# Optimization experiments

Hardware: AMD Instinct MI355X
Metric: run time of the kernel (lower is better)

Reference implementation:

```python
import jax, jax.numpy as jnp
import numpy as np

# Per-level grid spatial shapes: ceil([T,H,W]/grid_size/2**i) + 1 with
# video (T,H,W) = (120,1080,1920), grid_size=8, n_levels=2.
GRID_SHAPES = [jnp.array([16.0, 136.0, 241.0], dtype=jnp.float32),
               jnp.array([9.0, 69.0, 121.0], dtype=jnp.float32)]
EMB_DIM = 16
N_PTS = 1_000_000

# 8 binary corner offsets, MSB-first bit order (matches f'{i:03b}').
OFFSETS = jnp.array([[(i >> 2) & 1, (i >> 1) & 1, i & 1] for i in range(8)],
                    dtype=jnp.float32)  # [8,3]


def setup_inputs() -> dict:
    key = jax.random.key(0)
    k0, k1, k2 = jax.random.split(key, 3)
    inputs = jax.random.uniform(k0, (N_PTS, 3), dtype=jnp.float32)
    emb0 = jax.random.normal(k1, (16, 136, 241, EMB_DIM), dtype=jnp.float32)
    emb1 = jax.random.normal(k2, (9, 69, 121, EMB_DIM), dtype=jnp.float32)
    return {"inputs": inputs, "emb0": emb0, "emb1": emb1}


def _encode_level(inputs, emb, gshape):
    # inputs: [N,3] in [0,1]; emb: [T,H,W,D]; gshape: [3] float grid shape
    coords = inputs * (gshape - 1.0)                         # [N,3]
    corner = jnp.floor(coords[:, None, :] + OFFSETS)         # [N,8,3]
    corner = jnp.clip(corner, 0.0, gshape - 1.0)             # [N,8,3]
    idx = corner.astype(jnp.int32)
    values = emb[idx[..., 0], idx[..., 1], idx[..., 2]]      # [N,8,D] gather
    weights = jnp.prod(1.0 - jnp.abs(corner - coords[:, None, :]),
                       axis=-1, keepdims=True)               # [N,8,1]
    return jnp.sum(weights * values, axis=-2)                # [N,D]


def reference(inputs, emb0, emb1):
    out0 = _encode_level(inputs, emb0, GRID_SHAPES[0])
    out1 = _encode_level(inputs, emb1, GRID_SHAPES[1])
    return jnp.concatenate([out0, out1], axis=-1)            # [N, 2*D]
```

## Files before the change

kernel.cpp:

```cpp
#include <hip/hip_runtime.h>


typedef float floatx4 __attribute__((ext_vector_type(4)));

#define KXB 8
#define KYB 17
#define KZB 31
#define NBINS (KXB * KYB * KZB)
#define NSUB 4
#define CAPS 104
#define CAP_TOT (NSUB * CAPS)

#define L0X 3
#define L0Y 9
#define L0Z 9
#define L0CELLS (L0X * L0Y * L0Z)
#define L1X 3
#define L1Y 6
#define L1Z 5
#define L1CELLS (L1X * L1Y * L1Z)
#define CSTR 20

__device__ __forceinline__ int point_key(float px, float py, float pz) {
    int ix = (int)(px * 15.0f);  ix = min(max(ix, 0), 15);
    int iy = (int)(py * 135.0f); iy = min(max(iy, 0), 135);
    int iz = (int)(pz * 240.0f); iz = min(max(iz, 0), 240);
    return ((ix >> 1) * KYB + (iy >> 3)) * KZB + (iz >> 3);
}

__device__ __forceinline__ void load4pts(const float* __restrict__ pts, int i4,
                                         float px[4], float py[4], float pz[4]) {
    const floatx4* v = (const floatx4*)(pts + (size_t)i4 * 3);
    const floatx4 a = v[0], b = v[1], c = v[2];
    px[0] = a.x; py[0] = a.y; pz[0] = a.z;
    px[1] = a.w; py[1] = b.x; pz[1] = b.y;
    px[2] = b.z; py[2] = b.w; pz[2] = c.x;
    px[3] = c.y; py[3] = c.z; pz[3] = c.w;
}

__global__ __launch_bounds__(256)
void k_bin(const float* __restrict__ pts, int n,
           unsigned* __restrict__ cnt, unsigned* __restrict__ ovfc,
           unsigned* __restrict__ slots, unsigned* __restrict__ ovf) {
    const int i4 = (blockIdx.x * blockDim.x + threadIdx.x) * 4;
    if (i4 >= n) return;
    if (i4 + 3 < n) {
        float px[4], py[4], pz[4];
        load4pts(pts, i4, px, py, pz);
        int k[4];
#pragma unroll
        for (int j = 0; j < 4; ++j) k[j] = point_key(px[j], py[j], pz[j]);
        unsigned pos[4];
#pragma unroll
        for (int j = 0; j < 4; ++j)
            pos[j] = atomicAdd(&cnt[j * NBINS + k[j]], 1u);
#pragma unroll
        for (int j = 0; j < 4; ++j) {
            if (pos[j] < CAPS)
                slots[(size_t)k[j] * CAP_TOT + j * CAPS + pos[j]] = (unsigned)(i4 + j);
            else
                ovf[atomicAdd(ovfc, 1u)] = (unsigned)(i4 + j);
        }
    } else {
        for (int j = 0; j < 4 && i4 + j < n; ++j) {
            const size_t b = (size_t)(i4 + j) * 3;
            const int k = point_key(pts[b], pts[b+1], pts[b+2]);
            const unsigned pos = atomicAdd(&cnt[j * NBINS + k], 1u);
            if (pos < CAPS) slots[(size_t)k * CAP_TOT + j * CAPS + pos] = (unsigned)(i4 + j);
            else            ovf[atomicAdd(ovfc, 1u)] = (unsigned)(i4 + j);
        }
    }
}

__device__ __forceinline__ void setup_lds(float cx, float cy, float cz,
                                          float tm1, float hm1, float wm1,
                                          int xb, int yb, int zb,
                                          int ex, int ey, int ez,
                                          int sx, int sy, int d,
                                          int* __restrict__ off,
                                          float* __restrict__ w) {
    float gx[2] = { floorf(cx), floorf(cx + 1.0f) };
    float gy[2] = { floorf(cy), floorf(cy + 1.0f) };
    float gz[2] = { floorf(cz), floorf(cz + 1.0f) };
    float wx[2], wy[2], wz[2];
    int   xo[2], yo[2], zo[2];
#pragma unroll
    for (int b = 0; b < 2; ++b) {
        gx[b] = fminf(fmaxf(gx[b], 0.0f), tm1);
        gy[b] = fminf(fmaxf(gy[b], 0.0f), hm1);
        gz[b] = fminf(fmaxf(gz[b], 0.0f), wm1);
        wx[b] = 1.0f - fabsf(gx[b] - cx);
        wy[b] = 1.0f - fabsf(gy[b] - cy);
        wz[b] = 1.0f - fabsf(gz[b] - cz);
        xo[b] = min((int)gx[b] - xb, ex) * sx;
        yo[b] = min((int)gy[b] - yb, ey) * sy;
        zo[b] = min((int)gz[b] - zb, ez) * CSTR + d;
    }
    float wyz[4];
    int   yzo[4];
#pragma unroll
    for (int j = 0; j < 2; ++j)
#pragma unroll
        for (int k = 0; k < 2; ++k) {
            wyz[2 * j + k] = wy[j] * wz[k];
            yzo[2 * j + k] = yo[j] + zo[k];
        }
#pragma unroll
    for (int c = 0; c < 8; ++c) {
        const int i = (c >> 2) & 1, jk = c & 3;
        w[c]   = wx[i] * wyz[jk];
        off[c] = xo[i] + yzo[jk];
    }
}

__global__ __launch_bounds__(256)
void k_main_bins(const unsigned* __restrict__ slots,
                 const unsigned* __restrict__ cnt,
                 const float* __restrict__ pts,
                 const float* __restrict__ emb0,
                 const float* __restrict__ emb1,
                 float* __restrict__ out) {
    const int bin = (blockIdx.x & 7) * 527 + (blockIdx.x >> 3);
    const unsigned n0 = min(cnt[bin],             (unsigned)CAPS);
    const unsigned n1 = min(cnt[NBINS + bin],     (unsigned)CAPS);
    const unsigned n2 = min(cnt[2 * NBINS + bin], (unsigned)CAPS);
    const unsigned n3 = min(cnt[3 * NBINS + bin], (unsigned)CAPS);
    const unsigned c0 = n0, c1 = c0 + n1, c2 = c1 + n2, nt = c2 + n3;
    if (nt == 0) return;

    const int bz = bin % KZB;
    const int t1 = bin / KZB;
    const int by = t1 % KYB;
    const int bx = t1 / KYB;

    const int x0 = bx * 2, y0 = by * 8, z0 = bz * 8;
    const int x1b = bx, y1b = (544 * by) / 135, z1b = bz * 4;

    __shared__ float lds0[L0CELLS * CSTR];
    __shared__ float lds1[L1CELLS * CSTR];

    const int tid = threadIdx.x;
    for (int idx = tid; idx < L0CELLS * 4; idx += 256) {
        const int cell = idx >> 2, q = (idx & 3) * 4;
        const int lz = cell % L0Z;
        const int t = cell / L0Z;
        const int ly = t % L0Y, lx = t / L0Y;
        const int gx = min(x0 + lx, 15), gy = min(y0 + ly, 135), gz = min(z0 + lz, 240);
        const floatx4 v = *(const floatx4*)(emb0 + ((size_t)(gx * 136 + gy) * 241 + gz) * 16 + q);
        *(floatx4*)(lds0 + cell * CSTR + q) = v;
    }
    for (int idx = tid; idx < L1CELLS * 4; idx += 256) {
        const int cell = idx >> 2, q = (idx & 3) * 4;
        const int lz = cell % L1Z;
        const int t = cell / L1Z;
        const int ly = t % L1Y, lx = t / L1Y;
        const int gx = min(x1b + lx, 8), gy = min(y1b + ly, 68), gz = min(z1b + lz, 120);
        const floatx4 v = *(const floatx4*)(emb1 + ((size_t)(gx * 69 + gy) * 121 + gz) * 16 + q);
        *(floatx4*)(lds1 + cell * CSTR + q) = v;
    }
    __syncthreads();

    const int quad = tid >> 2;
    const int d = (tid & 3) * 4;
    const size_t sbase = (size_t)bin * CAP_TOT;

    auto slot_of = [&](unsigned t) -> unsigned {
        const unsigned seg = (t >= c0) + (t >= c1) + (t >= c2);
        const unsigned base = (seg == 0) ? 0u : ((seg == 1) ? c0 : ((seg == 2) ? c1 : c2));
        return (unsigned)(sbase + seg * CAPS + (t - base));
    };

    unsigned tA = quad, tB = quad + 64;
    int origA = (int)slots[slot_of(min(tA, nt - 1))];
    int origB = (int)slots[slot_of(min(tB, nt - 1))];
    size_t pbA = (size_t)origA * 3;
    float pxA = pts[pbA], pyA = pts[pbA + 1], pzA = pts[pbA + 2];

    while (tA < nt) {
        const unsigned tC = tB + 64;
        const int origC = (int)slots[slot_of(min(tC, nt - 1))];
        const size_t pbB = (size_t)origB * 3;
        const float pxB = pts[pbB], pyB = pts[pbB + 1], pzB = pts[pbB + 2];

        int   o0[8], o1[8];
        float w0[8], w1[8];
        setup_lds(pxA * 15.0f, pyA * 135.0f, pzA * 240.0f, 15.0f, 135.0f, 240.0f,
                  x0, y0, z0, L0X - 1, L0Y - 1, L0Z - 1,
                  L0Y * L0Z * CSTR, L0Z * CSTR, d, o0, w0);
        setup_lds(pxA * 8.0f, pyA * 68.0f, pzA * 120.0f, 8.0f, 68.0f, 120.0f,
                  x1b, y1b, z1b, L1X - 1, L1Y - 1, L1Z - 1,
                  L1Y * L1Z * CSTR, L1Z * CSTR, d, o1, w1);

        floatx4 a0 = {0.f, 0.f, 0.f, 0.f}, a1 = {0.f, 0.f, 0.f, 0.f};
#pragma unroll
        for (int c = 0; c < 8; ++c) a0 += w0[c] * *(const floatx4*)(lds0 + o0[c]);
#pragma unroll
        for (int c = 0; c < 8; ++c) a1 += w1[c] * *(const floatx4*)(lds1 + o1[c]);

        float* row = out + (size_t)origA * 32 + d;
        __builtin_nontemporal_store(a0, (floatx4*)row);
        __builtin_nontemporal_store(a1, (floatx4*)(row + 16));

        tA = tB; tB = tC;
        origA = origB; origB = origC;
        pxA = pxB; pyA = pyB; pzA = pzB;
    }
}

__device__ __forceinline__ void setup_glb(float cx, float cy, float cz,
                                          float tm1, float hm1, float wm1,
                                          int sh, int sw, int d,
                                          int* __restrict__ off,
                                          float* __restrict__ w) {
    float gx[2] = { floorf(cx), floorf(cx + 1.0f) };
    float gy[2] = { floorf(cy), floorf(cy + 1.0f) };
    float gz[2] = { floorf(cz), floorf(cz + 1.0f) };
    float wx[2], wy[2], wz[2];
    int   xo[2], yo[2], zo[2];
#pragma unroll
    for (int b = 0; b < 2; ++b) {
        gx[b] = fminf(fmaxf(gx[b], 0.0f), tm1);
        gy[b] = fminf(fmaxf(gy[b], 0.0f), hm1);
        gz[b] = fminf(fmaxf(gz[b], 0.0f), wm1);
        wx[b] = 1.0f - fabsf(gx[b] - cx);
        wy[b] = 1.0f - fabsf(gy[b] - cy);
        wz[b] = 1.0f - fabsf(gz[b] - cz);
        xo[b] = (int)gx[b] * sh;
        yo[b] = (int)gy[b] * sw;
        zo[b] = (int)gz[b] * 16 + d;
    }
    float wyz[4];
    int   yzo[4];
#pragma unroll
    for (int j = 0; j < 2; ++j)
#pragma unroll
        for (int k = 0; k < 2; ++k) {
            wyz[2 * j + k] = wy[j] * wz[k];
            yzo[2 * j + k] = yo[j] + zo[k];
        }
#pragma unroll
    for (int c = 0; c < 8; ++c) {
        const int i = (c >> 2) & 1, jk = c & 3;
        w[c]   = wx[i] * wyz[jk];
        off[c] = xo[i] + yzo[jk];
    }
}

__global__ __launch_bounds__(256)
void k_overflow(const unsigned* __restrict__ ovf, const unsigned* __restrict__ ovfc,
                const float* __restrict__ pts,
                const float* __restrict__ emb0, const float* __restrict__ emb1,
                float* __restrict__ out) {
    const unsigned total = *ovfc;
    const int lane4 = (int)(threadIdx.x & 3) * 4;
    for (unsigned i = (blockIdx.x * 256 + threadIdx.x) >> 2; i < total;
         i += (gridDim.x * 256) >> 2) {
        const int p = (int)ovf[i];
        const size_t b = (size_t)p * 3;
        const float px = pts[b], py = pts[b + 1], pz = pts[b + 2];
        int   o0[8], o1[8];
        float w0[8], w1[8];
        setup_glb(px * 15.0f, py * 135.0f, pz * 240.0f, 15.0f, 135.0f, 240.0f,
                  136 * 241 * 16, 241 * 16, lane4, o0, w0);
        setup_glb(px * 8.0f, py * 68.0f, pz * 120.0f, 8.0f, 68.0f, 120.0f,
                  69 * 121 * 16, 121 * 16, lane4, o1, w1);
        floatx4 a0 = {0,0,0,0}, a1 = {0,0,0,0};
#pragma unroll
        for (int c = 0; c < 8; ++c) a0 += w0[c] * *(const floatx4*)(emb0 + o0[c]);
#pragma unroll
        for (int c = 0; c < 8; ++c) a1 += w1[c] * *(const floatx4*)(emb1 + o1[c]);
        float* row = out + (size_t)p * 32 + lane4;
        __builtin_nontemporal_store(a0, (floatx4*)row);
        __builtin_nontemporal_store(a1, (floatx4*)(row + 16));
    }
}

__global__ __launch_bounds__(256)
void k_main_plain(const float* __restrict__ pts,
                  const float* __restrict__ emb0,
                  const float* __restrict__ emb1,
                  float* __restrict__ out, int n) {
    const int g = blockIdx.x * blockDim.x + threadIdx.x;
    const int p = g >> 2;
    const int d = (g & 3) * 4;
    if (p >= n) return;
    const size_t b = (size_t)p * 3;
    const float px = pts[b], py = pts[b + 1], pz = pts[b + 2];
    int   o0[8], o1[8];
    float w0[8], w1[8];
    setup_glb(px * 15.0f, py * 135.0f, pz * 240.0f, 15.0f, 135.0f, 240.0f,
              136 * 241 * 16, 241 * 16, d, o0, w0);
    setup_glb(px * 8.0f, py * 68.0f, pz * 120.0f, 8.0f, 68.0f, 120.0f,
              69 * 121 * 16, 121 * 16, d, o1, w1);
    floatx4 a0 = {0,0,0,0}, a1 = {0,0,0,0};
#pragma unroll
    for (int c = 0; c < 8; ++c) a0 += w0[c] * *(const floatx4*)(emb0 + o0[c]);
#pragma unroll
    for (int c = 0; c < 8; ++c) a1 += w1[c] * *(const floatx4*)(emb1 + o1[c]);
    float* row = out + (size_t)p * 32 + d;
    __builtin_nontemporal_store(a0, (floatx4*)row);
    __builtin_nontemporal_store(a1, (floatx4*)(row + 16));
}

extern "C" void kernel_launch(void* const* d_in, const int* in_sizes, int n_in,
                              void* d_out, int out_size, void* d_ws, size_t ws_size,
                              hipStream_t stream) {
    const float* pts  = (const float*)d_in[0];
    const float* emb0 = (const float*)d_in[1];
    const float* emb1 = (const float*)d_in[2];
    float* out = (float*)d_out;
    const int n = in_sizes[0] / 3;

    const int block = 256;
    const int n4      = (n + 3) / 4;
    const int grid_p4 = (n4 + block - 1) / block;
    const int grid_4l = (int)(((long long)n * 4 + block - 1) / block);

    const size_t off_cnt   = 0;
    const size_t off_ovfc  = (size_t)NSUB * NBINS * 4;
    const size_t off_slots = ((off_ovfc + 4 + 31) & ~(size_t)31);
    const size_t off_ovf   = off_slots + (size_t)NBINS * CAP_TOT * 4;
    const size_t need      = off_ovf + (size_t)n * 4;

    if (ws_size < need) {
        k_main_plain<<<grid_4l, block, 0, stream>>>(pts, emb0, emb1, out, n);
        return;
    }

    char* ws = (char*)d_ws;
    unsigned* cnt   = (unsigned*)(ws + off_cnt);
    unsigned* ovfc  = (unsigned*)(ws + off_ovfc);
    unsigned* slots = (unsigned*)(ws + off_slots);
    unsigned* ovf   = (unsigned*)(ws + off_ovf);

    hipMemsetAsync(cnt, 0, off_ovfc + 4, stream);
    k_bin<<<grid_p4, block, 0, stream>>>(pts, n, cnt, ovfc, slots, ovf);
    k_main_bins<<<NBINS, block, 0, stream>>>(slots, cnt, pts, emb0, emb1, out);
    k_overflow<<<64, block, 0, stream>>>(ovf, ovfc, pts, emb0, emb1, out);
}
```

Before: 118.4 us.

## Fuse overflow pass into bin kernel, replace memset, pad LDS stride to 17

```diff
diff --git a/kernel.cpp b/kernel.cpp
--- a/kernel.cpp
+++ b/kernel.cpp
@@ -10,6 +10,7 @@
 #define NSUB 4
 #define CAPS 104
 #define CAP_TOT (NSUB * CAPS)
+#define CNT_DWORDS (NSUB * NBINS + 1)
 
 #define L0X 3
 #define L0Y 9
@@ -19,7 +20,7 @@
 #define L1Y 6
 #define L1Z 5
 #define L1CELLS (L1X * L1Y * L1Z)
-#define CSTR 20
+#define CSTR 17
 
 __device__ __forceinline__ int point_key(float px, float py, float pz) {
     int ix = (int)(px * 15.0f);  ix = min(max(ix, 0), 15);
@@ -36,6 +37,12 @@
     px[1] = a.w; py[1] = b.x; pz[1] = b.y;
     px[2] = b.z; py[2] = b.w; pz[2] = c.x;
     px[3] = c.y; py[3] = c.z; pz[3] = c.w;
+}
+
+__global__ __launch_bounds__(256)
+void k_zero(unsigned* __restrict__ cnt) {
+    const int i = blockIdx.x * blockDim.x + threadIdx.x;
+    if (i < CNT_DWORDS) cnt[i] = 0u;
 }
 
 __global__ __launch_bounds__(256)
@@ -113,9 +120,73 @@
     }
 }
 
-__global__ __launch_bounds__(256)
+__device__ __forceinline__ void setup_glb(float cx, float cy, float cz,
+                                          float tm1, float hm1, float wm1,
+                                          int sh, int sw, int d,
+                                          int* __restrict__ off,
+                                          float* __restrict__ w) {
+    float gx[2] = { floorf(cx), floorf(cx + 1.0f) };
+    float gy[2] = { floorf(cy), floorf(cy + 1.0f) };
+    float gz[2] = { floorf(cz), floorf(cz + 1.0f) };
+    float wx[2], wy[2], wz[2];
+    int   xo[2], yo[2], zo[2];
+#pragma unroll
+    for (int b = 0; b < 2; ++b) {
+        gx[b] = fminf(fmaxf(gx[b], 0.0f), tm1);
+        gy[b] = fminf(fmaxf(gy[b], 0.0f), hm1);
+        gz[b] = fminf(fmaxf(gz[b], 0.0f), wm1);
+        wx[b] = 1.0f - fabsf(gx[b] - cx);
+        wy[b] = 1.0f - fabsf(gy[b] - cy);
+        wz[b] = 1.0f - fabsf(gz[b] - cz);
+        xo[b] = (int)gx[b] * sh;
+        yo[b] = (int)gy[b] * sw;
+        zo[b] = (int)gz[b] * 16 + d;
+    }
+    float wyz[4];
+    int   yzo[4];
+#pragma unroll
+    for (int j = 0; j < 2; ++j)
+#pragma unroll
+        for (int k = 0; k < 2; ++k) {
+            wyz[2 * j + k] = wy[j] * wz[k];
+            yzo[2 * j + k] = yo[j] + zo[k];
+        }
+#pragma unroll
+    for (int c = 0; c < 8; ++c) {
+        const int i = (c >> 2) & 1, jk = c & 3;
+        w[c]   = wx[i] * wyz[jk];
+        off[c] = xo[i] + yzo[jk];
+    }
+}
+
+__device__ __forceinline__ void encode_glb_quad(int p, int lane4,
+                                                const float* __restrict__ pts,
+                                                const float* __restrict__ emb0,
+                                                const float* __restrict__ emb1,
+                                                float* __restrict__ out) {
+    const size_t b = (size_t)p * 3;
+    const float px = pts[b], py = pts[b + 1], pz = pts[b + 2];
+    int   o0[8], o1[8];
+    float w0[8], w1[8];
+    setup_glb(px * 15.0f, py * 135.0f, pz * 240.0f, 15.0f, 135.0f, 240.0f,
+              136 * 241 * 16, 241 * 16, lane4, o0, w0);
+    setup_glb(px * 8.0f, py * 68.0f, pz * 120.0f, 8.0f, 68.0f, 120.0f,
+              69 * 121 * 16, 121 * 16, lane4, o1, w1);
+    floatx4 a0 = {0,0,0,0}, a1 = {0,0,0,0};
+#pragma unroll
+    for (int c = 0; c < 8; ++c) a0 += w0[c] * *(const floatx4*)(emb0 + o0[c]);
+#pragma unroll
+    for (int c = 0; c < 8; ++c) a1 += w1[c] * *(const floatx4*)(emb1 + o1[c]);
+    float* row = out + (size_t)p * 32 + lane4;
+    __builtin_nontemporal_store(a0, (floatx4*)row);
+    __builtin_nontemporal_store(a1, (floatx4*)(row + 16));
+}
+
+__global__ __launch_bounds__(256, 6)
 void k_main_bins(const unsigned* __restrict__ slots,
                  const unsigned* __restrict__ cnt,
+                 const unsigned* __restrict__ ovfc,
+                 const unsigned* __restrict__ ovf,
                  const float* __restrict__ pts,
                  const float* __restrict__ emb0,
                  const float* __restrict__ emb1,
@@ -126,152 +197,94 @@
     const unsigned n2 = min(cnt[2 * NBINS + bin], (unsigned)CAPS);
     const unsigned n3 = min(cnt[3 * NBINS + bin], (unsigned)CAPS);
     const unsigned c0 = n0, c1 = c0 + n1, c2 = c1 + n2, nt = c2 + n3;
-    if (nt == 0) return;
-
-    const int bz = bin % KZB;
-    const int t1 = bin / KZB;
-    const int by = t1 % KYB;
-    const int bx = t1 / KYB;
-
-    const int x0 = bx * 2, y0 = by * 8, z0 = bz * 8;
-    const int x1b = bx, y1b = (544 * by) / 135, z1b = bz * 4;
 
     __shared__ float lds0[L0CELLS * CSTR];
     __shared__ float lds1[L1CELLS * CSTR];
 
     const int tid = threadIdx.x;
-    for (int idx = tid; idx < L0CELLS * 4; idx += 256) {
-        const int cell = idx >> 2, q = (idx & 3) * 4;
-        const int lz = cell % L0Z;
-        const int t = cell / L0Z;
-        const int ly = t % L0Y, lx = t / L0Y;
-        const int gx = min(x0 + lx, 15), gy = min(y0 + ly, 135), gz = min(z0 + lz, 240);
-        const floatx4 v = *(const floatx4*)(emb0 + ((size_t)(gx * 136 + gy) * 241 + gz) * 16 + q);
-        *(floatx4*)(lds0 + cell * CSTR + q) = v;
-    }
-    for (int idx = tid; idx < L1CELLS * 4; idx += 256) {
-        const int cell = idx >> 2, q = (idx & 3) * 4;
-        const int lz = cell % L1Z;
-        const int t = cell / L1Z;
-        const int ly = t % L1Y, lx = t / L1Y;
-        const int gx = min(x1b + lx, 8), gy = min(y1b + ly, 68), gz = min(z1b + lz, 120);
-        const floatx4 v = *(const floatx4*)(emb1 + ((size_t)(gx * 69 + gy) * 121 + gz) * 16 + q);
-        *(floatx4*)(lds1 + cell * CSTR + q) = v;
-    }
-    __syncthreads();
-
-    const int quad = tid >> 2;
     const int d = (tid & 3) * 4;
-    const size_t sbase = (size_t)bin * CAP_TOT;
-
-    auto slot_of = [&](unsigned t) -> unsigned {
-        const unsigned seg = (t >= c0) + (t >= c1) + (t >= c2);
-        const unsigned base = (seg == 0) ? 0u : ((seg == 1) ? c0 : ((seg == 2) ? c1 : c2));
-        return (unsigned)(sbase + seg * CAPS + (t - base));
-    };
-
-    unsigned tA = quad, tB = quad + 64;
-    int origA = (int)slots[slot_of(min(tA, nt - 1))];
-    int origB = (int)slots[slot_of(min(tB, nt - 1))];
-    size_t pbA = (size_t)origA * 3;
-    float pxA = pts[pbA], pyA = pts[pbA + 1], pzA = pts[pbA + 2];
-
-    while (tA < nt) {
-        const unsigned tC = tB + 64;
-        const int origC = (int)slots[slot_of(min(tC, nt - 1))];
-        const size_t pbB = (size_t)origB * 3;
-        const float pxB = pts[pbB], pyB = pts[pbB + 1], pzB = pts[pbB + 2];
-
-        int   o0[8], o1[8];
-        float w0[8], w1[8];
-        setup_lds(pxA * 15.0f, pyA * 135.0f, pzA * 240.0f, 15.0f, 135.0f, 240.0f,
-                  x0, y0, z0, L0X - 1, L0Y - 1, L0Z - 1,
-                  L0Y * L0Z * CSTR, L0Z * CSTR, d, o0, w0);
-        setup_lds(pxA * 8.0f, pyA * 68.0f, pzA * 120.0f, 8.0f, 68.0f, 120.0f,
-                  x1b, y1b, z1b, L1X - 1, L1Y - 1, L1Z - 1,
-                  L1Y * L1Z * CSTR, L1Z * CSTR, d, o1, w1);
-
-        floatx4 a0 = {0.f, 0.f, 0.f, 0.f}, a1 = {0.f, 0.f, 0.f, 0.f};
-#pragma unroll
-        for (int c = 0; c < 8; ++c) a0 += w0[c] * *(const floatx4*)(lds0 + o0[c]);
-#pragma unroll
-        for (int c = 0; c < 8; ++c) a1 += w1[c] * *(const floatx4*)(lds1 + o1[c]);
-
-        float* row = out + (size_t)origA * 32 + d;
-        __builtin_nontemporal_store(a0, (floatx4*)row);
-        __builtin_nontemporal_store(a1, (floatx4*)(row + 16));
-
-        tA = tB; tB = tC;
-        origA = origB; origB = origC;
-        pxA = pxB; pyA = pyB; pzA = pzB;
-    }
-}
-
-__device__ __forceinline__ void setup_glb(float cx, float cy, float cz,
-                                          float tm1, float hm1, float wm1,
-                                          int sh, int sw, int d,
-                                          int* __restrict__ off,
-                                          float* __restrict__ w) {
-    float gx[2] = { floorf(cx), floorf(cx + 1.0f) };
-    float gy[2] = { floorf(cy), floorf(cy + 1.0f) };
-    float gz[2] = { floorf(cz), floorf(cz + 1.0f) };
-    float wx[2], wy[2], wz[2];
-    int   xo[2], yo[2], zo[2];
-#pragma unroll
-    for (int b = 0; b < 2; ++b) {
-        gx[b] = fminf(fmaxf(gx[b], 0.0f), tm1);
-        gy[b] = fminf(fmaxf(gy[b], 0.0f), hm1);
-        gz[b] = fminf(fmaxf(gz[b], 0.0f), wm1);
-        wx[b] = 1.0f - fabsf(gx[b] - cx);
-        wy[b] = 1.0f - fabsf(gy[b] - cy);
-        wz[b] = 1.0f - fabsf(gz[b] - cz);
-        xo[b] = (int)gx[b] * sh;
-        yo[b] = (int)gy[b] * sw;
-        zo[b] = (int)gz[b] * 16 + d;
-    }
-    float wyz[4];
-    int   yzo[4];
-#pragma unroll
-    for (int j = 0; j < 2; ++j)
-#pragma unroll
-        for (int k = 0; k < 2; ++k) {
-            wyz[2 * j + k] = wy[j] * wz[k];
-            yzo[2 * j + k] = yo[j] + zo[k];
-        }
-#pragma unroll
-    for (int c = 0; c < 8; ++c) {
-        const int i = (c >> 2) & 1, jk = c & 3;
-        w[c]   = wx[i] * wyz[jk];
-        off[c] = xo[i] + yzo[jk];
-    }
-}
-
-__global__ __launch_bounds__(256)
-void k_overflow(const unsigned* __restrict__ ovf, const unsigned* __restrict__ ovfc,
-                const float* __restrict__ pts,
-                const float* __restrict__ emb0, const float* __restrict__ emb1,
-                float* __restrict__ out) {
-    const unsigned total = *ovfc;
-    const int lane4 = (int)(threadIdx.x & 3) * 4;
-    for (unsigned i = (blockIdx.x * 256 + threadIdx.x) >> 2; i < total;
-         i += (gridDim.x * 256) >> 2) {
-        const int p = (int)ovf[i];
-        const size_t b = (size_t)p * 3;
-        const float px = pts[b], py = pts[b + 1], pz = pts[b + 2];
-        int   o0[8], o1[8];
-        float w0[8], w1[8];
-        setup_glb(px * 15.0f, py * 135.0f, pz * 240.0f, 15.0f, 135.0f, 240.0f,
-                  136 * 241 * 16, 241 * 16, lane4, o0, w0);
-        setup_glb(px * 8.0f, py * 68.0f, pz * 120.0f, 8.0f, 68.0f, 120.0f,
-                  69 * 121 * 16, 121 * 16, lane4, o1, w1);
-        floatx4 a0 = {0,0,0,0}, a1 = {0,0,0,0};
-#pragma unroll
-        for (int c = 0; c < 8; ++c) a0 += w0[c] * *(const floatx4*)(emb0 + o0[c]);
-#pragma unroll
-        for (int c = 0; c < 8; ++c) a1 += w1[c] * *(const floatx4*)(emb1 + o1[c]);
-        float* row = out + (size_t)p * 32 + lane4;
-        __builtin_nontemporal_store(a0, (floatx4*)row);
-        __builtin_nontemporal_store(a1, (floatx4*)(row + 16));
+
+    if (nt != 0) {
+        const int bz = bin % KZB;
+        const int t1 = bin / KZB;
+        const int by = t1 % KYB;
+        const int bx = t1 / KYB;
+
+        const int x0 = bx * 2, y0 = by * 8, z0 = bz * 8;
+        const int x1b = bx, y1b = (544 * by) / 135, z1b = bz * 4;
+
+        for (int idx = tid; idx < L0CELLS * 4; idx += 256) {
+            const int cell = idx >> 2, q = (idx & 3) * 4;
+            const int lz = cell % L0Z;
+            const int t = cell / L0Z;
+            const int ly = t % L0Y, lx = t / L0Y;
+            const int gx = min(x0 + lx, 15), gy = min(y0 + ly, 135), gz = min(z0 + lz, 240);
+            const floatx4 v = *(const floatx4*)(emb0 + ((size_t)(gx * 136 + gy) * 241 + gz) * 16 + q);
+            *(floatx4*)(lds0 + cell * CSTR + q) = v;
+        }
+        for (int idx = tid; idx < L1CELLS * 4; idx += 256) {
+            const int cell = idx >> 2, q = (idx & 3) * 4;
+            const int lz = cell % L1Z;
+            const int t = cell / L1Z;
+            const int ly = t % L1Y, lx = t / L1Y;
+            const int gx = min(x1b + lx, 8), gy = min(y1b + ly, 68), gz = min(z1b + lz, 120);
+            const floatx4 v = *(const floatx4*)(emb1 + ((size_t)(gx * 69 + gy) * 121 + gz) * 16 + q);
+            *(floatx4*)(lds1 + cell * CSTR + q) = v;
+        }
+        __syncthreads();
+
+        const int quad = tid >> 2;
+        const size_t sbase = (size_t)bin * CAP_TOT;
+
+        auto slot_of = [&](unsigned t) -> unsigned {
+            const unsigned seg = (t >= c0) + (t >= c1) + (t >= c2);
+            const unsigned base = (seg == 0) ? 0u : ((seg == 1) ? c0 : ((seg == 2) ? c1 : c2));
+            return (unsigned)(sbase + seg * CAPS + (t - base));
+        };
+
+        unsigned tA = quad, tB = quad + 64;
+        int origA = (int)slots[slot_of(min(tA, nt - 1))];
+        int origB = (int)slots[slot_of(min(tB, nt - 1))];
+        size_t pbA = (size_t)origA * 3;
+        float pxA = pts[pbA], pyA = pts[pbA + 1], pzA = pts[pbA + 2];
+
+        while (tA < nt) {
+            const unsigned tC = tB + 64;
+            const int origC = (int)slots[slot_of(min(tC, nt - 1))];
+            const size_t pbB = (size_t)origB * 3;
+            const float pxB = pts[pbB], pyB = pts[pbB + 1], pzB = pts[pbB + 2];
+
+            int   o0[8], o1[8];
+            float w0[8], w1[8];
+            setup_lds(pxA * 15.0f, pyA * 135.0f, pzA * 240.0f, 15.0f, 135.0f, 240.0f,
+                      x0, y0, z0, L0X - 1, L0Y - 1, L0Z - 1,
+                      L0Y * L0Z * CSTR, L0Z * CSTR, d, o0, w0);
+            setup_lds(pxA * 8.0f, pyA * 68.0f, pzA * 120.0f, 8.0f, 68.0f, 120.0f,
+                      x1b, y1b, z1b, L1X - 1, L1Y - 1, L1Z - 1,
+                      L1Y * L1Z * CSTR, L1Z * CSTR, d, o1, w1);
+
+            floatx4 a0 = {0.f, 0.f, 0.f, 0.f}, a1 = {0.f, 0.f, 0.f, 0.f};
+#pragma unroll
+            for (int c = 0; c < 8; ++c) a0 += w0[c] * *(const floatx4*)(lds0 + o0[c]);
+#pragma unroll
+            for (int c = 0; c < 8; ++c) a1 += w1[c] * *(const floatx4*)(lds1 + o1[c]);
+
+            float* row = out + (size_t)origA * 32 + d;
+            __builtin_nontemporal_store(a0, (floatx4*)row);
+            __builtin_nontemporal_store(a1, (floatx4*)(row + 16));
+
+            tA = tB; tB = tC;
+            origA = origB; origB = origC;
+            pxA = pxB; pyA = pyB; pzA = pzB;
+        }
+    }
+
+    if (blockIdx.x < 64) {
+        const unsigned total = *ovfc;
+        for (unsigned i = (blockIdx.x * 256 + tid) >> 2; i < total;
+             i += (64u * 256u) >> 2) {
+            encode_glb_quad((int)ovf[i], d, pts, emb0, emb1, out);
+        }
     }
 }
 
@@ -282,24 +295,8 @@
                   float* __restrict__ out, int n) {
     const int g = blockIdx.x * blockDim.x + threadIdx.x;
     const int p = g >> 2;
-    const int d = (g & 3) * 4;
     if (p >= n) return;
-    const size_t b = (size_t)p * 3;
-    const float px = pts[b], py = pts[b + 1], pz = pts[b + 2];
-    int   o0[8], o1[8];
-    float w0[8], w1[8];
-    setup_glb(px * 15.0f, py * 135.0f, pz * 240.0f, 15.0f, 135.0f, 240.0f,
-              136 * 241 * 16, 241 * 16, d, o0, w0);
-    setup_glb(px * 8.0f, py * 68.0f, pz * 120.0f, 8.0f, 68.0f, 120.0f,
-              69 * 121 * 16, 121 * 16, d, o1, w1);
-    floatx4 a0 = {0,0,0,0}, a1 = {0,0,0,0};
-#pragma unroll
-    for (int c = 0; c < 8; ++c) a0 += w0[c] * *(const floatx4*)(emb0 + o0[c]);
-#pragma unroll
-    for (int c = 0; c < 8; ++c) a1 += w1[c] * *(const floatx4*)(emb1 + o1[c]);
-    float* row = out + (size_t)p * 32 + d;
-    __builtin_nontemporal_store(a0, (floatx4*)row);
-    __builtin_nontemporal_store(a1, (floatx4*)(row + 16));
+    encode_glb_quad(p, (g & 3) * 4, pts, emb0, emb1, out);
 }
 
 extern "C" void kernel_launch(void* const* d_in, const int* in_sizes, int n_in,
@@ -315,6 +312,7 @@
     const int n4      = (n + 3) / 4;
     const int grid_p4 = (n4 + block - 1) / block;
     const int grid_4l = (int)(((long long)n * 4 + block - 1) / block);
+    const int grid_z  = (CNT_DWORDS + block - 1) / block;
 
     const size_t off_cnt   = 0;
     const size_t off_ovfc  = (size_t)NSUB * NBINS * 4;
@@ -333,8 +331,8 @@
     unsigned* slots = (unsigned*)(ws + off_slots);
     unsigned* ovf   = (unsigned*)(ws + off_ovf);
 
-    hipMemsetAsync(cnt, 0, off_ovfc + 4, stream);
+    k_zero<<<grid_z, block, 0, stream>>>(cnt);
     k_bin<<<grid_p4, block, 0, stream>>>(pts, n, cnt, ovfc, slots, ovf);
-    k_main_bins<<<NBINS, block, 0, stream>>>(slots, cnt, pts, emb0, emb1, out);
-    k_overflow<<<64, block, 0, stream>>>(ovf, ovfc, pts, emb0, emb1, out);
-}
+    k_main_bins<<<NBINS, block, 0, stream>>>(slots, cnt, ovfc, ovf,
+                                             pts, emb0, emb1, out);
+}
```

Result: faster. 115.1 us (-2.8%).
